# Kernel optimization log

Measured on AMD Instinct MI355X. Metric: run time of the kernel, lower is better.

The kernel has to match this reference:

```python
import jax, jax.numpy as jnp
import numpy as np

DIM = 2048
NUM_HEADS = 16
NUM_KV_HEADS = 4
HEAD_DIM = DIM // NUM_HEADS  # 128, even (RoPE requirement)
MAX_DEPTH = 16
ROPE_BASE = 10000.0
EPS = 1.1920929e-07  # torch F.rms_norm default eps = fp32 machine eps
SCALE = 1.0 / float(np.sqrt(HEAD_DIM))

# Precomputed bidirectional RoPE tables (buffers in the torch module)
_inv_freq = 1.0 / ROPE_BASE ** (np.arange(0, HEAD_DIM, 2, dtype=np.float32) / HEAD_DIM)
_pos = np.arange(MAX_DEPTH, dtype=np.float32)
_rpos = np.arange(MAX_DEPTH - 1, -1, -1, dtype=np.float32)
_fw = np.outer(_pos, _inv_freq)
_rv = np.outer(_rpos, _inv_freq)
DEPTH_COS = jnp.asarray(np.cos(_fw))   # [MAX_DEPTH, HEAD_DIM//2]
DEPTH_SIN = jnp.asarray(np.sin(_fw))
REV_COS = jnp.asarray(np.cos(_rv))
REV_SIN = jnp.asarray(np.sin(_rv))


def _rmsnorm(t):
    return t * jax.lax.rsqrt(jnp.mean(t * t, axis=-1, keepdims=True) + EPS)


def setup_inputs() -> dict:
    key = jax.random.key(0)
    ks = jax.random.split(key, 7)
    B, S, DH = 4, 2048, 7  # depth = DH + 1 = 8 <= MAX_DEPTH
    kv_dim = NUM_KV_HEADS * HEAD_DIM
    return {
        "x": jax.random.normal(ks[0], (B, S, DIM), jnp.float32),
        "depth_history": jax.random.normal(ks[1], (B, S, DH, DIM), jnp.float32),
        "Wq": jax.random.normal(ks[2], (DIM, DIM), jnp.float32) * 0.02,
        "Wk": jax.random.normal(ks[3], (kv_dim, DIM), jnp.float32) * 0.02,
        "Wv": jax.random.normal(ks[4], (kv_dim, DIM), jnp.float32) * 0.02,
        "Wproj": jax.random.normal(ks[5], (DIM, DIM), jnp.float32) * 0.02,
        "q_gain": jnp.full((NUM_HEADS,), 1.0, jnp.float32),
    }


def reference(x, depth_history, Wq, Wk, Wv, Wproj, q_gain):
    B, S, D = x.shape
    # torch.stack([*depth_history, x], dim=2) -> [B, S, depth, D]
    kv_source = jnp.concatenate([depth_history, x[:, :, None, :]], axis=2)
    depth = kv_source.shape[2]
    N = B * S
    half = HEAD_DIM // 2

    q = (x @ Wq.T).reshape(N, 1, NUM_HEADS, HEAD_DIM).transpose(0, 2, 1, 3)          # [N,H,1,hd]
    k = (kv_source @ Wk.T).reshape(N, depth, NUM_KV_HEADS, HEAD_DIM).transpose(0, 2, 1, 3)  # [N,Hkv,depth,hd]
    v = (kv_source @ Wv.T).reshape(N, depth, NUM_KV_HEADS, HEAD_DIM).transpose(0, 2, 1, 3)

    q = _rmsnorm(q)
    k = _rmsnorm(k)

    q1, q2 = q[..., :half], q[..., half:]
    k1, k2 = k[..., :half], k[..., half:]
    # query uses position depth-1 of each table; keys use positions 0..depth-1
    qc, qs = DEPTH_COS[depth - 1], DEPTH_SIN[depth - 1]        # [half]
    rqc, rqs = REV_COS[depth - 1], REV_SIN[depth - 1]
    kc, ksn = DEPTH_COS[:depth], DEPTH_SIN[:depth]             # [depth, half]
    rkc, rks = REV_COS[:depth], REV_SIN[:depth]

    q = jnp.concatenate([q1 * qc + q2 * qs, -q1 * rqs + q2 * rqc], axis=-1)
    k = jnp.concatenate([k1 * kc + k2 * ksn, -k1 * rks + k2 * rkc], axis=-1)

    q = q * q_gain[None, :, None, None]

    # GQA: replicate kv heads to match query heads
    group = NUM_HEADS // NUM_KV_HEADS
    k = jnp.repeat(k, group, axis=1)
    v = jnp.repeat(v, group, axis=1)

    scores = jnp.einsum('nhqd,nhkd->nhqk', q, k) * SCALE       # [N,H,1,depth]
    attn = jax.nn.softmax(scores, axis=-1)
    y = jnp.einsum('nhqk,nhkd->nhqd', attn, v)                 # [N,H,1,hd]
    y = y.transpose(0, 2, 1, 3).reshape(B, S, D)
    return y @ Wproj.T
```

## Files before the change

### kernel.cpp

```cpp
#include <hip/hip_runtime.h>
#include <cstdint>
#include <cstddef>

#define NTOK   8192
#define DIMM   2048
#define KVD    512
#define NHEAD  16
#define NKVH   4
#define HDIM   128
#define NDEPTH 8
#define EPSI   1.1920929e-07f
#define QSCALE 0.08838834764831845f
#define NLN64  (-0.14391156831212787f)
#define LDA    40

typedef __attribute__((ext_vector_type(8))) short bf16x8;
typedef __attribute__((ext_vector_type(4))) float f32x4;

__device__ __forceinline__ unsigned short f2bf(float f) {
  union { float f; unsigned int u; } v; v.f = f;
  unsigned int u = v.u;
  return (unsigned short)((u + 0x7fffu + ((u >> 16) & 1u)) >> 16);
}
__device__ __forceinline__ float bf2f(unsigned short h) {
  union { unsigned int u; float f; } v; v.u = ((unsigned int)h) << 16;
  return v.f;
}
__device__ __forceinline__ f32x4 mfma16(bf16x8 a, bf16x8 b, f32x4 c) {
  return __builtin_amdgcn_mfma_f32_16x16x32_bf16(a, b, c, 0, 0, 0);
}

__global__ __launch_bounds__(256) void cvt_kernel(const float* __restrict__ in,
                                                  unsigned short* __restrict__ out, int n4) {
  int i = blockIdx.x * 256 + threadIdx.x;
  if (i < n4) {
    float4 f = *(const float4*)(in + (size_t)i * 4);
    *(ushort4*)(out + (size_t)i * 4) = make_ushort4(f2bf(f.x), f2bf(f.y), f2bf(f.z), f2bf(f.w));
  }
}

__global__ __launch_bounds__(256, 2)
void gemm_q_kernel(const float* __restrict__ X, const unsigned short* __restrict__ W,
                   const float* __restrict__ QG, unsigned short* __restrict__ Q) {
  __shared__ unsigned short lA[128 * LDA];
  __shared__ unsigned short lB[128 * LDA];
  const int t = threadIdx.x;
  const int lane = t & 63, w = t >> 6;
  const int m = lane & 15, q4 = lane >> 4;
  const int row0 = blockIdx.y * 128;
  const int h = blockIdx.x;
  const int col0 = h * 128;

  f32x4 acc[2][8];
#pragma unroll
  for (int i = 0; i < 2; ++i)
#pragma unroll
    for (int j = 0; j < 8; ++j) acc[i][j] = (f32x4){0.f, 0.f, 0.f, 0.f};

  const float* aptr[4]; const unsigned short* bptr[4]; int dst[4];
#pragma unroll
  for (int it = 0; it < 4; ++it) {
    int idx = t + it * 256;
    int r = idx >> 3, c = (idx & 7) * 4;
    aptr[it] = X + (size_t)(row0 + r) * DIMM + c;
    bptr[it] = W + (size_t)(col0 + r) * DIMM + c;
    dst[it] = r * LDA + c;
  }
  for (int kt = 0; kt < DIMM; kt += 32) {
#pragma unroll
    for (int it = 0; it < 4; ++it) {
      float4 f = *(const float4*)(aptr[it] + kt);
      *(ushort4*)&lA[dst[it]] = make_ushort4(f2bf(f.x), f2bf(f.y), f2bf(f.z), f2bf(f.w));
      *(ushort4*)&lB[dst[it]] = *(const ushort4*)(bptr[it] + kt);
    }
    __syncthreads();
    const int ao = (w * 32 + m) * LDA + q4 * 8;
    bf16x8 a0 = *(const bf16x8*)&lA[ao];
    bf16x8 a1 = *(const bf16x8*)&lA[ao + 16 * LDA];
#pragma unroll
    for (int j = 0; j < 8; ++j) {
      bf16x8 b = *(const bf16x8*)&lB[(j * 16 + m) * LDA + q4 * 8];
      acc[0][j] = mfma16(a0, b, acc[0][j]);
      acc[1][j] = mfma16(a1, b, acc[1][j]);
    }
    __syncthreads();
  }
  const float gain = QG[h] * QSCALE;
#pragma unroll
  for (int i = 0; i < 2; ++i)
#pragma unroll
    for (int r = 0; r < 4; ++r) {
      float ss = 0.f;
#pragma unroll
      for (int j = 0; j < 8; ++j) { float vv = acc[i][j][r]; ss += vv * vv; }
      ss += __shfl_xor(ss, 1); ss += __shfl_xor(ss, 2);
      ss += __shfl_xor(ss, 4); ss += __shfl_xor(ss, 8);
      const float sc = rsqrtf(ss * (1.0f / 128.0f) + EPSI);
      const int gr = row0 + w * 32 + i * 16 + q4 * 4 + r;
      unsigned short* op = Q + (size_t)gr * DIMM + col0;
#pragma unroll
      for (int j = 0; j < 4; ++j) {
        const int c = j * 16 + m;
        const float inv = __expf((float)c * NLN64);
        float s1, c1, s2, c2;
        __sincosf(7.0f * inv, &s1, &c1);
        __sincosf(8.0f * inv, &s2, &c2);
        const float n1 = acc[i][j][r] * sc;
        const float n2 = acc[i][j + 4][r] * sc;
        op[c]      = f2bf((n1 * c1 + n2 * s1) * gain);
        op[c + 64] = f2bf((n2 * c2 - n1 * s2) * gain);
      }
    }
}

__global__ __launch_bounds__(256, 2)
void gemm_kv_kernel(const float* __restrict__ X, const float* __restrict__ DH,
                    const unsigned short* __restrict__ WK, const unsigned short* __restrict__ WV,
                    unsigned short* __restrict__ K, unsigned short* __restrict__ V) {
  __shared__ unsigned short lA[128 * LDA];
  __shared__ unsigned short lBk[128 * LDA];
  __shared__ unsigned short lBv[128 * LDA];
  const int t = threadIdx.x;
  const int lane = t & 63, w = t >> 6;
  const int m = lane & 15, q4 = lane >> 4;
  const int row0 = blockIdx.y * 128;
  const int col0 = blockIdx.x * 128;

  f32x4 acck[2][8], accv[2][8];
#pragma unroll
  for (int i = 0; i < 2; ++i)
#pragma unroll
    for (int j = 0; j < 8; ++j) { acck[i][j] = (f32x4){0.f,0.f,0.f,0.f}; accv[i][j] = (f32x4){0.f,0.f,0.f,0.f}; }

  const float* aptr[4]; const unsigned short* kptr[4]; const unsigned short* vptr[4]; int dst[4];
#pragma unroll
  for (int it = 0; it < 4; ++it) {
    int idx = t + it * 256;
    int r = idx >> 3, c = (idx & 7) * 4;
    int gr = row0 + r;
    int n = gr >> 3, d = gr & 7;
    aptr[it] = (d == 7) ? (X + (size_t)n * DIMM + c) : (DH + ((size_t)n * 7 + d) * DIMM + c);
    kptr[it] = WK + (size_t)(col0 + r) * DIMM + c;
    vptr[it] = WV + (size_t)(col0 + r) * DIMM + c;
    dst[it] = r * LDA + c;
  }
  for (int kt = 0; kt < DIMM; kt += 32) {
#pragma unroll
    for (int it = 0; it < 4; ++it) {
      float4 f = *(const float4*)(aptr[it] + kt);
      *(ushort4*)&lA[dst[it]]  = make_ushort4(f2bf(f.x), f2bf(f.y), f2bf(f.z), f2bf(f.w));
      *(ushort4*)&lBk[dst[it]] = *(const ushort4*)(kptr[it] + kt);
      *(ushort4*)&lBv[dst[it]] = *(const ushort4*)(vptr[it] + kt);
    }
    __syncthreads();
    const int ao = (w * 32 + m) * LDA + q4 * 8;
    bf16x8 a0 = *(const bf16x8*)&lA[ao];
    bf16x8 a1 = *(const bf16x8*)&lA[ao + 16 * LDA];
#pragma unroll
    for (int j = 0; j < 8; ++j) {
      const int bo = (j * 16 + m) * LDA + q4 * 8;
      bf16x8 bk = *(const bf16x8*)&lBk[bo];
      acck[0][j] = mfma16(a0, bk, acck[0][j]);
      acck[1][j] = mfma16(a1, bk, acck[1][j]);
      bf16x8 bv = *(const bf16x8*)&lBv[bo];
      accv[0][j] = mfma16(a0, bv, accv[0][j]);
      accv[1][j] = mfma16(a1, bv, accv[1][j]);
    }
    __syncthreads();
  }
#pragma unroll
  for (int i = 0; i < 2; ++i)
#pragma unroll
    for (int r = 0; r < 4; ++r) {
      const int gr = row0 + w * 32 + i * 16 + q4 * 4 + r;
      unsigned short* vp = V + (size_t)gr * KVD + col0;
#pragma unroll
      for (int j = 0; j < 8; ++j) vp[j * 16 + m] = f2bf(accv[i][j][r]);
      float ss = 0.f;
#pragma unroll
      for (int j = 0; j < 8; ++j) { float vv = acck[i][j][r]; ss += vv * vv; }
      ss += __shfl_xor(ss, 1); ss += __shfl_xor(ss, 2);
      ss += __shfl_xor(ss, 4); ss += __shfl_xor(ss, 8);
      const float sc = rsqrtf(ss * (1.0f / 128.0f) + EPSI);
      const int d = gr & 7;
      const float fd = (float)d, fr = (float)(15 - d);
      unsigned short* kp = K + (size_t)gr * KVD + col0;
#pragma unroll
      for (int j = 0; j < 4; ++j) {
        const int c = j * 16 + m;
        const float inv = __expf((float)c * NLN64);
        float s1, c1, s2, c2;
        __sincosf(fd * inv, &s1, &c1);
        __sincosf(fr * inv, &s2, &c2);
        const float n1 = acck[i][j][r] * sc;
        const float n2 = acck[i][j + 4][r] * sc;
        kp[c]      = f2bf(n1 * c1 + n2 * s1);
        kp[c + 64] = f2bf(n2 * c2 - n1 * s2);
      }
    }
}

__global__ __launch_bounds__(256)
void attn_kernel(const unsigned short* __restrict__ Q, const unsigned short* __restrict__ K,
                 const unsigned short* __restrict__ V, unsigned short* __restrict__ Y) {
  __shared__ unsigned short lK[NDEPTH * KVD];
  __shared__ unsigned short lV[NDEPTH * KVD];
  const int n = blockIdx.x;
  const int t = threadIdx.x;
#pragma unroll
  for (int i = 0; i < 4; ++i) {
    int idx = t * 4 + i * 1024;
    *(ushort4*)&lK[idx] = *(const ushort4*)&K[(size_t)n * (NDEPTH * KVD) + idx];
    *(ushort4*)&lV[idx] = *(const ushort4*)&V[(size_t)n * (NDEPTH * KVD) + idx];
  }
  __syncthreads();
  const int h = t >> 4, sub = t & 15;
  const int c0 = sub * 8;
  const int hk = h >> 2;
  const unsigned short* qp = Q + (size_t)n * DIMM + h * HDIM + c0;
  ushort4 qa = *(const ushort4*)qp;
  ushort4 qb = *(const ushort4*)(qp + 4);
  float qv[8] = {bf2f(qa.x), bf2f(qa.y), bf2f(qa.z), bf2f(qa.w),
                 bf2f(qb.x), bf2f(qb.y), bf2f(qb.z), bf2f(qb.w)};
  float s[NDEPTH];
#pragma unroll
  for (int d = 0; d < NDEPTH; ++d) {
    const unsigned short* kp = &lK[d * KVD + hk * HDIM + c0];
    ushort4 ka = *(const ushort4*)kp;
    ushort4 kb = *(const ushort4*)(kp + 4);
    float p = qv[0]*bf2f(ka.x) + qv[1]*bf2f(ka.y) + qv[2]*bf2f(ka.z) + qv[3]*bf2f(ka.w)
            + qv[4]*bf2f(kb.x) + qv[5]*bf2f(kb.y) + qv[6]*bf2f(kb.z) + qv[7]*bf2f(kb.w);
    p += __shfl_xor(p, 1); p += __shfl_xor(p, 2);
    p += __shfl_xor(p, 4); p += __shfl_xor(p, 8);
    s[d] = p;
  }
  float mx = s[0];
#pragma unroll
  for (int d = 1; d < NDEPTH; ++d) mx = fmaxf(mx, s[d]);
  float sum = 0.f;
#pragma unroll
  for (int d = 0; d < NDEPTH; ++d) { s[d] = __expf(s[d] - mx); sum += s[d]; }
  const float rs = 1.0f / sum;
  float yv[8] = {0.f,0.f,0.f,0.f,0.f,0.f,0.f,0.f};
#pragma unroll
  for (int d = 0; d < NDEPTH; ++d) {
    const float p = s[d] * rs;
    const unsigned short* vp = &lV[d * KVD + hk * HDIM + c0];
    ushort4 va = *(const ushort4*)vp;
    ushort4 vb = *(const ushort4*)(vp + 4);
    yv[0] += p*bf2f(va.x); yv[1] += p*bf2f(va.y); yv[2] += p*bf2f(va.z); yv[3] += p*bf2f(va.w);
    yv[4] += p*bf2f(vb.x); yv[5] += p*bf2f(vb.y); yv[6] += p*bf2f(vb.z); yv[7] += p*bf2f(vb.w);
  }
  unsigned short* yp = Y + (size_t)n * DIMM + h * HDIM + c0;
  *(ushort4*)yp       = make_ushort4(f2bf(yv[0]), f2bf(yv[1]), f2bf(yv[2]), f2bf(yv[3]));
  *(ushort4*)(yp + 4) = make_ushort4(f2bf(yv[4]), f2bf(yv[5]), f2bf(yv[6]), f2bf(yv[7]));
}

__global__ __launch_bounds__(256, 2)
void gemm_proj_kernel(const unsigned short* __restrict__ Yb, const unsigned short* __restrict__ W,
                      float* __restrict__ OUT) {
  __shared__ unsigned short lA[128 * LDA];
  __shared__ unsigned short lB[128 * LDA];
  const int t = threadIdx.x;
  const int lane = t & 63, w = t >> 6;
  const int m = lane & 15, q4 = lane >> 4;
  const int row0 = blockIdx.y * 128;
  const int col0 = blockIdx.x * 128;

  f32x4 acc[2][8];
#pragma unroll
  for (int i = 0; i < 2; ++i)
#pragma unroll
    for (int j = 0; j < 8; ++j) acc[i][j] = (f32x4){0.f, 0.f, 0.f, 0.f};

  const unsigned short* aptr[4]; const unsigned short* bptr[4]; int dst[4];
#pragma unroll
  for (int it = 0; it < 4; ++it) {
    int idx = t + it * 256;
    int r = idx >> 3, c = (idx & 7) * 4;
    aptr[it] = Yb + (size_t)(row0 + r) * DIMM + c;
    bptr[it] = W + (size_t)(col0 + r) * DIMM + c;
    dst[it] = r * LDA + c;
  }
  for (int kt = 0; kt < DIMM; kt += 32) {
#pragma unroll
    for (int it = 0; it < 4; ++it) {
      *(ushort4*)&lA[dst[it]] = *(const ushort4*)(aptr[it] + kt);
      *(ushort4*)&lB[dst[it]] = *(const ushort4*)(bptr[it] + kt);
    }
    __syncthreads();
    const int ao = (w * 32 + m) * LDA + q4 * 8;
    bf16x8 a0 = *(const bf16x8*)&lA[ao];
    bf16x8 a1 = *(const bf16x8*)&lA[ao + 16 * LDA];
#pragma unroll
    for (int j = 0; j < 8; ++j) {
      bf16x8 b = *(const bf16x8*)&lB[(j * 16 + m) * LDA + q4 * 8];
      acc[0][j] = mfma16(a0, b, acc[0][j]);
      acc[1][j] = mfma16(a1, b, acc[1][j]);
    }
    __syncthreads();
  }
#pragma unroll
  for (int i = 0; i < 2; ++i)
#pragma unroll
    for (int r = 0; r < 4; ++r) {
      const int gr = row0 + w * 32 + i * 16 + q4 * 4 + r;
      float* op = OUT + (size_t)gr * DIMM + col0;
#pragma unroll
      for (int j = 0; j < 8; ++j) op[j * 16 + m] = acc[i][j][r];
    }
}

extern "C" void kernel_launch(void* const* d_in, const int* in_sizes, int n_in,
                              void* d_out, int out_size, void* d_ws, size_t ws_size,
                              hipStream_t stream) {
  const float* x  = (const float*)d_in[0];
  const float* dh = (const float*)d_in[1];
  const float* Wq = (const float*)d_in[2];
  const float* Wk = (const float*)d_in[3];
  const float* Wv = (const float*)d_in[4];
  const float* Wp = (const float*)d_in[5];
  const float* qg = (const float*)d_in[6];
  float* out = (float*)d_out;
  char* ws = (char*)d_ws;

  unsigned short* wq_b = (unsigned short*)(ws + 0);
  unsigned short* wk_b = (unsigned short*)(ws + 8388608);
  unsigned short* wv_b = (unsigned short*)(ws + 10485760);
  unsigned short* wp_b = (unsigned short*)(ws + 12582912);
  unsigned short* q_b  = (unsigned short*)(ws + 20971520);
  unsigned short* k_b  = (unsigned short*)(ws + 54525952);
  unsigned short* v_b  = (unsigned short*)(ws + 121634816);
  unsigned short* y_b  = (unsigned short*)(ws + 188743680);

  cvt_kernel<<<4096, 256, 0, stream>>>(Wq, wq_b, 1048576);
  cvt_kernel<<<1024, 256, 0, stream>>>(Wk, wk_b, 262144);
  cvt_kernel<<<1024, 256, 0, stream>>>(Wv, wv_b, 262144);
  cvt_kernel<<<4096, 256, 0, stream>>>(Wp, wp_b, 1048576);

  gemm_q_kernel<<<dim3(16, 64), 256, 0, stream>>>(x, wq_b, qg, q_b);
  gemm_kv_kernel<<<dim3(4, 512), 256, 0, stream>>>(x, dh, wk_b, wv_b, k_b, v_b);
  attn_kernel<<<8192, 256, 0, stream>>>(q_b, k_b, v_b, y_b);
  gemm_proj_kernel<<<dim3(16, 64), 256, 0, stream>>>(y_b, wp_b, out);
}
```

Baseline: 1.366 ms.

## Use direct global-to-LDS loads and larger per-wave tiles in GEMMs

The bf16 weight and activation tiles now go straight from global memory to LDS through global_load_lds, without staging in registers, and the LDS row padding is removed. The Q and projection GEMMs move to 256x128 block tiles, so each wave computes a 64x128 output. The KV GEMM now splits waves 2x2 and combines the RMSnorm partial sums through shared memory. The goals are more MFMA work per LDS read and less load-instruction overhead. The cost is more accumulator registers, possible LDS bank conflicts from the unpadded stride-32 layout, and fewer blocks in flight.

```diff
diff --git a/kernel.cpp b/kernel.cpp
--- a/kernel.cpp
+++ b/kernel.cpp
@@ -6,13 +6,11 @@
 #define DIMM   2048
 #define KVD    512
 #define NHEAD  16
-#define NKVH   4
 #define HDIM   128
 #define NDEPTH 8
 #define EPSI   1.1920929e-07f
 #define QSCALE 0.08838834764831845f
 #define NLN64  (-0.14391156831212787f)
-#define LDA    40
 
 typedef __attribute__((ext_vector_type(8))) short bf16x8;
 typedef __attribute__((ext_vector_type(4))) float f32x4;
@@ -28,6 +26,11 @@
 }
 __device__ __forceinline__ f32x4 mfma16(bf16x8 a, bf16x8 b, f32x4 c) {
   return __builtin_amdgcn_mfma_f32_16x16x32_bf16(a, b, c, 0, 0, 0);
+}
+__device__ __forceinline__ void gl_lds16(const unsigned short* g, unsigned short* l) {
+  __builtin_amdgcn_global_load_lds((const __attribute__((address_space(1))) unsigned int*)g,
+                                   (__attribute__((address_space(3))) unsigned int*)l,
+                                   16, 0, 0);
 }
 
 __global__ __launch_bounds__(256) void cvt_kernel(const float* __restrict__ in,
@@ -42,52 +45,57 @@
 __global__ __launch_bounds__(256, 2)
 void gemm_q_kernel(const float* __restrict__ X, const unsigned short* __restrict__ W,
                    const float* __restrict__ QG, unsigned short* __restrict__ Q) {
-  __shared__ unsigned short lA[128 * LDA];
-  __shared__ unsigned short lB[128 * LDA];
-  const int t = threadIdx.x;
-  const int lane = t & 63, w = t >> 6;
+  __shared__ unsigned short lA[256 * 32];
+  __shared__ unsigned short lB[128 * 32];
+  const int t = threadIdx.x, lane = t & 63, w = t >> 6;
   const int m = lane & 15, q4 = lane >> 4;
-  const int row0 = blockIdx.y * 128;
-  const int h = blockIdx.x;
-  const int col0 = h * 128;
-
-  f32x4 acc[2][8];
-#pragma unroll
-  for (int i = 0; i < 2; ++i)
+  const int row0 = blockIdx.y * 256, h = blockIdx.x, col0 = h * 128;
+
+  f32x4 acc[4][8];
+#pragma unroll
+  for (int i = 0; i < 4; ++i)
 #pragma unroll
     for (int j = 0; j < 8; ++j) acc[i][j] = (f32x4){0.f, 0.f, 0.f, 0.f};
 
-  const float* aptr[4]; const unsigned short* bptr[4]; int dst[4];
-#pragma unroll
-  for (int it = 0; it < 4; ++it) {
-    int idx = t + it * 256;
-    int r = idx >> 3, c = (idx & 7) * 4;
-    aptr[it] = X + (size_t)(row0 + r) * DIMM + c;
-    bptr[it] = W + (size_t)(col0 + r) * DIMM + c;
-    dst[it] = r * LDA + c;
-  }
+  const int ra = t >> 1, ca = (t & 1) * 16;
+  const int rb = t >> 2, cb = (t & 3) * 8;
+
+  const float* asrc0 = X + (size_t)(row0 + ra) * DIMM + ca;
+  const float* asrc1 = X + (size_t)(row0 + 128 + ra) * DIMM + ca;
+  const unsigned short* bsrc0 = W + (size_t)(col0 + rb) * DIMM + cb;
+  const unsigned short* bsrc1 = W + (size_t)(col0 + rb + 64) * DIMM + cb;
+
   for (int kt = 0; kt < DIMM; kt += 32) {
-#pragma unroll
-    for (int it = 0; it < 4; ++it) {
-      float4 f = *(const float4*)(aptr[it] + kt);
-      *(ushort4*)&lA[dst[it]] = make_ushort4(f2bf(f.x), f2bf(f.y), f2bf(f.z), f2bf(f.w));
-      *(ushort4*)&lB[dst[it]] = *(const ushort4*)(bptr[it] + kt);
-    }
-    __syncthreads();
-    const int ao = (w * 32 + m) * LDA + q4 * 8;
-    bf16x8 a0 = *(const bf16x8*)&lA[ao];
-    bf16x8 a1 = *(const bf16x8*)&lA[ao + 16 * LDA];
+    gl_lds16(bsrc0 + kt, &lB[(size_t)t * 8]);
+    gl_lds16(bsrc1 + kt, &lB[((size_t)t + 256) * 8]);
+#pragma unroll
+    for (int i = 0; i < 2; ++i) {
+      const float* src = (i == 0 ? asrc0 : asrc1) + kt;
+      float4 f0 = *(const float4*)(src);
+      float4 f1 = *(const float4*)(src + 4);
+      float4 f2 = *(const float4*)(src + 8);
+      float4 f3 = *(const float4*)(src + 12);
+      unsigned short* dst = &lA[(i * 128 + ra) * 32 + ca];
+      ((ushort4*)dst)[0] = make_ushort4(f2bf(f0.x), f2bf(f0.y), f2bf(f0.z), f2bf(f0.w));
+      ((ushort4*)dst)[1] = make_ushort4(f2bf(f1.x), f2bf(f1.y), f2bf(f1.z), f2bf(f1.w));
+      ((ushort4*)dst)[2] = make_ushort4(f2bf(f2.x), f2bf(f2.y), f2bf(f2.z), f2bf(f2.w));
+      ((ushort4*)dst)[3] = make_ushort4(f2bf(f3.x), f2bf(f3.y), f2bf(f3.z), f2bf(f3.w));
+    }
+    __syncthreads();
+    bf16x8 a[4];
+#pragma unroll
+    for (int i = 0; i < 4; ++i) a[i] = *(const bf16x8*)&lA[(w * 64 + i * 16 + m) * 32 + q4 * 8];
 #pragma unroll
     for (int j = 0; j < 8; ++j) {
-      bf16x8 b = *(const bf16x8*)&lB[(j * 16 + m) * LDA + q4 * 8];
-      acc[0][j] = mfma16(a0, b, acc[0][j]);
-      acc[1][j] = mfma16(a1, b, acc[1][j]);
+      bf16x8 b = *(const bf16x8*)&lB[(j * 16 + m) * 32 + q4 * 8];
+#pragma unroll
+      for (int i = 0; i < 4; ++i) acc[i][j] = mfma16(a[i], b, acc[i][j]);
     }
     __syncthreads();
   }
   const float gain = QG[h] * QSCALE;
 #pragma unroll
-  for (int i = 0; i < 2; ++i)
+  for (int i = 0; i < 4; ++i)
 #pragma unroll
     for (int r = 0; r < 4; ++r) {
       float ss = 0.f;
@@ -96,7 +104,7 @@
       ss += __shfl_xor(ss, 1); ss += __shfl_xor(ss, 2);
       ss += __shfl_xor(ss, 4); ss += __shfl_xor(ss, 8);
       const float sc = rsqrtf(ss * (1.0f / 128.0f) + EPSI);
-      const int gr = row0 + w * 32 + i * 16 + q4 * 4 + r;
+      const int gr = row0 + w * 64 + i * 16 + q4 * 4 + r;
       unsigned short* op = Q + (size_t)gr * DIMM + col0;
 #pragma unroll
       for (int j = 0; j < 4; ++j) {
@@ -117,83 +125,103 @@
 void gemm_kv_kernel(const float* __restrict__ X, const float* __restrict__ DH,
                     const unsigned short* __restrict__ WK, const unsigned short* __restrict__ WV,
                     unsigned short* __restrict__ K, unsigned short* __restrict__ V) {
-  __shared__ unsigned short lA[128 * LDA];
-  __shared__ unsigned short lBk[128 * LDA];
-  __shared__ unsigned short lBv[128 * LDA];
-  const int t = threadIdx.x;
-  const int lane = t & 63, w = t >> 6;
+  __shared__ unsigned short lA[128 * 32];
+  __shared__ unsigned short lBk[128 * 32];
+  __shared__ unsigned short lBv[128 * 32];
+  __shared__ float red[128 * 2];
+  const int t = threadIdx.x, lane = t & 63, w = t >> 6;
   const int m = lane & 15, q4 = lane >> 4;
-  const int row0 = blockIdx.y * 128;
-  const int col0 = blockIdx.x * 128;
-
-  f32x4 acck[2][8], accv[2][8];
-#pragma unroll
-  for (int i = 0; i < 2; ++i)
-#pragma unroll
-    for (int j = 0; j < 8; ++j) { acck[i][j] = (f32x4){0.f,0.f,0.f,0.f}; accv[i][j] = (f32x4){0.f,0.f,0.f,0.f}; }
-
-  const float* aptr[4]; const unsigned short* kptr[4]; const unsigned short* vptr[4]; int dst[4];
-#pragma unroll
-  for (int it = 0; it < 4; ++it) {
-    int idx = t + it * 256;
-    int r = idx >> 3, c = (idx & 7) * 4;
-    int gr = row0 + r;
-    int n = gr >> 3, d = gr & 7;
-    aptr[it] = (d == 7) ? (X + (size_t)n * DIMM + c) : (DH + ((size_t)n * 7 + d) * DIMM + c);
-    kptr[it] = WK + (size_t)(col0 + r) * DIMM + c;
-    vptr[it] = WV + (size_t)(col0 + r) * DIMM + c;
-    dst[it] = r * LDA + c;
-  }
+  const int wr = w >> 1, wc = w & 1;
+  const int row0 = blockIdx.y * 128, col0 = blockIdx.x * 128;
+
+  f32x4 acck[4][4], accv[4][4];
+#pragma unroll
+  for (int i = 0; i < 4; ++i)
+#pragma unroll
+    for (int j = 0; j < 4; ++j) { acck[i][j] = (f32x4){0.f,0.f,0.f,0.f}; accv[i][j] = (f32x4){0.f,0.f,0.f,0.f}; }
+
+  const int ra = t >> 1, ca = (t & 1) * 16;
+  const int rb = t >> 2, cb = (t & 3) * 8;
+  const int gra = row0 + ra, an = gra >> 3, ad = gra & 7;
+  const float* asrc = ((ad == 7) ? (X + (size_t)an * DIMM) : (DH + ((size_t)an * 7 + ad) * DIMM)) + ca;
+  const unsigned short* bk0 = WK + (size_t)(col0 + rb) * DIMM + cb;
+  const unsigned short* bk1 = WK + (size_t)(col0 + rb + 64) * DIMM + cb;
+  const unsigned short* bv0 = WV + (size_t)(col0 + rb) * DIMM + cb;
+  const unsigned short* bv1 = WV + (size_t)(col0 + rb + 64) * DIMM + cb;
+
   for (int kt = 0; kt < DIMM; kt += 32) {
-#pragma unroll
-    for (int it = 0; it < 4; ++it) {
-      float4 f = *(const float4*)(aptr[it] + kt);
-      *(ushort4*)&lA[dst[it]]  = make_ushort4(f2bf(f.x), f2bf(f.y), f2bf(f.z), f2bf(f.w));
-      *(ushort4*)&lBk[dst[it]] = *(const ushort4*)(kptr[it] + kt);
-      *(ushort4*)&lBv[dst[it]] = *(const ushort4*)(vptr[it] + kt);
-    }
-    __syncthreads();
-    const int ao = (w * 32 + m) * LDA + q4 * 8;
-    bf16x8 a0 = *(const bf16x8*)&lA[ao];
-    bf16x8 a1 = *(const bf16x8*)&lA[ao + 16 * LDA];
-#pragma unroll
-    for (int j = 0; j < 8; ++j) {
-      const int bo = (j * 16 + m) * LDA + q4 * 8;
-      bf16x8 bk = *(const bf16x8*)&lBk[bo];
-      acck[0][j] = mfma16(a0, bk, acck[0][j]);
-      acck[1][j] = mfma16(a1, bk, acck[1][j]);
-      bf16x8 bv = *(const bf16x8*)&lBv[bo];
-      accv[0][j] = mfma16(a0, bv, accv[0][j]);
-      accv[1][j] = mfma16(a1, bv, accv[1][j]);
-    }
-    __syncthreads();
-  }
-#pragma unroll
-  for (int i = 0; i < 2; ++i)
+    gl_lds16(bk0 + kt, &lBk[(size_t)t * 8]);
+    gl_lds16(bk1 + kt, &lBk[((size_t)t + 256) * 8]);
+    gl_lds16(bv0 + kt, &lBv[(size_t)t * 8]);
+    gl_lds16(bv1 + kt, &lBv[((size_t)t + 256) * 8]);
+    {
+      const float* src = asrc + kt;
+      float4 f0 = *(const float4*)(src);
+      float4 f1 = *(const float4*)(src + 4);
+      float4 f2 = *(const float4*)(src + 8);
+      float4 f3 = *(const float4*)(src + 12);
+      unsigned short* dst = &lA[ra * 32 + ca];
+      ((ushort4*)dst)[0] = make_ushort4(f2bf(f0.x), f2bf(f0.y), f2bf(f0.z), f2bf(f0.w));
+      ((ushort4*)dst)[1] = make_ushort4(f2bf(f1.x), f2bf(f1.y), f2bf(f1.z), f2bf(f1.w));
+      ((ushort4*)dst)[2] = make_ushort4(f2bf(f2.x), f2bf(f2.y), f2bf(f2.z), f2bf(f2.w));
+      ((ushort4*)dst)[3] = make_ushort4(f2bf(f3.x), f2bf(f3.y), f2bf(f3.z), f2bf(f3.w));
+    }
+    __syncthreads();
+    bf16x8 a[4];
+#pragma unroll
+    for (int i = 0; i < 4; ++i) a[i] = *(const bf16x8*)&lA[(wr * 64 + i * 16 + m) * 32 + q4 * 8];
+#pragma unroll
+    for (int j = 0; j < 4; ++j) {
+      const int T = wc * 2 + j + (j & 2);
+      bf16x8 bk = *(const bf16x8*)&lBk[(T * 16 + m) * 32 + q4 * 8];
+      bf16x8 bv = *(const bf16x8*)&lBv[(T * 16 + m) * 32 + q4 * 8];
+#pragma unroll
+      for (int i = 0; i < 4; ++i) {
+        acck[i][j] = mfma16(a[i], bk, acck[i][j]);
+        accv[i][j] = mfma16(a[i], bv, accv[i][j]);
+      }
+    }
+    __syncthreads();
+  }
+#pragma unroll
+  for (int i = 0; i < 4; ++i)
 #pragma unroll
     for (int r = 0; r < 4; ++r) {
-      const int gr = row0 + w * 32 + i * 16 + q4 * 4 + r;
+      const int lr = wr * 64 + i * 16 + q4 * 4 + r;
+      const int gr = row0 + lr;
       unsigned short* vp = V + (size_t)gr * KVD + col0;
 #pragma unroll
-      for (int j = 0; j < 8; ++j) vp[j * 16 + m] = f2bf(accv[i][j][r]);
+      for (int j = 0; j < 4; ++j) {
+        const int T = wc * 2 + j + (j & 2);
+        vp[T * 16 + m] = f2bf(accv[i][j][r]);
+      }
       float ss = 0.f;
 #pragma unroll
-      for (int j = 0; j < 8; ++j) { float vv = acck[i][j][r]; ss += vv * vv; }
+      for (int j = 0; j < 4; ++j) { float vv = acck[i][j][r]; ss += vv * vv; }
       ss += __shfl_xor(ss, 1); ss += __shfl_xor(ss, 2);
       ss += __shfl_xor(ss, 4); ss += __shfl_xor(ss, 8);
-      const float sc = rsqrtf(ss * (1.0f / 128.0f) + EPSI);
+      if (m == 0) red[lr * 2 + wc] = ss;
+    }
+  __syncthreads();
+#pragma unroll
+  for (int i = 0; i < 4; ++i)
+#pragma unroll
+    for (int r = 0; r < 4; ++r) {
+      const int lr = wr * 64 + i * 16 + q4 * 4 + r;
+      const int gr = row0 + lr;
+      const float sc = rsqrtf((red[lr * 2] + red[lr * 2 + 1]) * (1.0f / 128.0f) + EPSI);
       const int d = gr & 7;
       const float fd = (float)d, fr = (float)(15 - d);
       unsigned short* kp = K + (size_t)gr * KVD + col0;
 #pragma unroll
-      for (int j = 0; j < 4; ++j) {
-        const int c = j * 16 + m;
+      for (int j = 0; j < 2; ++j) {
+        const int c = (wc * 2 + j) * 16 + m;
         const float inv = __expf((float)c * NLN64);
         float s1, c1, s2, c2;
         __sincosf(fd * inv, &s1, &c1);
         __sincosf(fr * inv, &s2, &c2);
         const float n1 = acck[i][j][r] * sc;
-        const float n2 = acck[i][j + 4][r] * sc;
+        const float n2 = acck[i][j + 2][r] * sc;
         kp[c]      = f2bf(n1 * c1 + n2 * s1);
         kp[c + 64] = f2bf(n2 * c2 - n1 * s2);
       }
@@ -259,52 +287,45 @@
 __global__ __launch_bounds__(256, 2)
 void gemm_proj_kernel(const unsigned short* __restrict__ Yb, const unsigned short* __restrict__ W,
                       float* __restrict__ OUT) {
-  __shared__ unsigned short lA[128 * LDA];
-  __shared__ unsigned short lB[128 * LDA];
-  const int t = threadIdx.x;
-  const int lane = t & 63, w = t >> 6;
+  __shared__ unsigned short lA[256 * 32];
+  __shared__ unsigned short lB[128 * 32];
+  const int t = threadIdx.x, lane = t & 63, w = t >> 6;
   const int m = lane & 15, q4 = lane >> 4;
-  const int row0 = blockIdx.y * 128;
-  const int col0 = blockIdx.x * 128;
-
-  f32x4 acc[2][8];
-#pragma unroll
-  for (int i = 0; i < 2; ++i)
+  const int row0 = blockIdx.y * 256, col0 = blockIdx.x * 128;
+
+  f32x4 acc[4][8];
+#pragma unroll
+  for (int i = 0; i < 4; ++i)
 #pragma unroll
     for (int j = 0; j < 8; ++j) acc[i][j] = (f32x4){0.f, 0.f, 0.f, 0.f};
 
-  const unsigned short* aptr[4]; const unsigned short* bptr[4]; int dst[4];
-#pragma unroll
-  for (int it = 0; it < 4; ++it) {
-    int idx = t + it * 256;
-    int r = idx >> 3, c = (idx & 7) * 4;
-    aptr[it] = Yb + (size_t)(row0 + r) * DIMM + c;
-    bptr[it] = W + (size_t)(col0 + r) * DIMM + c;
-    dst[it] = r * LDA + c;
-  }
+  const int rb = t >> 2, cb = (t & 3) * 8;
+  const unsigned short* as0 = Yb + (size_t)(row0 + rb) * DIMM + cb;
+  const unsigned short* bs0 = W + (size_t)(col0 + rb) * DIMM + cb;
+
   for (int kt = 0; kt < DIMM; kt += 32) {
 #pragma unroll
-    for (int it = 0; it < 4; ++it) {
-      *(ushort4*)&lA[dst[it]] = *(const ushort4*)(aptr[it] + kt);
-      *(ushort4*)&lB[dst[it]] = *(const ushort4*)(bptr[it] + kt);
-    }
-    __syncthreads();
-    const int ao = (w * 32 + m) * LDA + q4 * 8;
-    bf16x8 a0 = *(const bf16x8*)&lA[ao];
-    bf16x8 a1 = *(const bf16x8*)&lA[ao + 16 * LDA];
+    for (int i = 0; i < 4; ++i)
+      gl_lds16(as0 + (size_t)i * 64 * DIMM + kt, &lA[((size_t)t + i * 256) * 8]);
+    gl_lds16(bs0 + kt, &lB[(size_t)t * 8]);
+    gl_lds16(bs0 + (size_t)64 * DIMM + kt, &lB[((size_t)t + 256) * 8]);
+    __syncthreads();
+    bf16x8 a[4];
+#pragma unroll
+    for (int i = 0; i < 4; ++i) a[i] = *(const bf16x8*)&lA[(w * 64 + i * 16 + m) * 32 + q4 * 8];
 #pragma unroll
     for (int j = 0; j < 8; ++j) {
-      bf16x8 b = *(const bf16x8*)&lB[(j * 16 + m) * LDA + q4 * 8];
-      acc[0][j] = mfma16(a0, b, acc[0][j]);
-      acc[1][j] = mfma16(a1, b, acc[1][j]);
-    }
-    __syncthreads();
-  }
-#pragma unroll
-  for (int i = 0; i < 2; ++i)
+      bf16x8 b = *(const bf16x8*)&lB[(j * 16 + m) * 32 + q4 * 8];
+#pragma unroll
+      for (int i = 0; i < 4; ++i) acc[i][j] = mfma16(a[i], b, acc[i][j]);
+    }
+    __syncthreads();
+  }
+#pragma unroll
+  for (int i = 0; i < 4; ++i)
 #pragma unroll
     for (int r = 0; r < 4; ++r) {
-      const int gr = row0 + w * 32 + i * 16 + q4 * 4 + r;
+      const int gr = row0 + w * 64 + i * 16 + q4 * 4 + r;
       float* op = OUT + (size_t)gr * DIMM + col0;
 #pragma unroll
       for (int j = 0; j < 8; ++j) op[j * 16 + m] = acc[i][j][r];
@@ -338,8 +359,8 @@
   cvt_kernel<<<1024, 256, 0, stream>>>(Wv, wv_b, 262144);
   cvt_kernel<<<4096, 256, 0, stream>>>(Wp, wp_b, 1048576);
 
-  gemm_q_kernel<<<dim3(16, 64), 256, 0, stream>>>(x, wq_b, qg, q_b);
+  gemm_q_kernel<<<dim3(16, 32), 256, 0, stream>>>(x, wq_b, qg, q_b);
   gemm_kv_kernel<<<dim3(4, 512), 256, 0, stream>>>(x, dh, wk_b, wv_b, k_b, v_b);
   attn_kernel<<<8192, 256, 0, stream>>>(q_b, k_b, v_b, y_b);
-  gemm_proj_kernel<<<dim3(16, 64), 256, 0, stream>>>(y_b, wp_b, out);
-}
+  gemm_proj_kernel<<<dim3(16, 32), 256, 0, stream>>>(y_b, wp_b, out);
+}
```

Measured after the change: 1.325 ms. -3.1%, faster.
